# Optimization experiments

Measured on AMD Instinct MI355X. Metric: run time of the kernel, lower is better.

The kernel has to match this reference:

```python
import jax, jax.numpy as jnp
from jax import lax
import numpy as np

KSIZE = 3      # match-patch size
STRIDE = 1
RATE = 2       # down/up-sampling rate
FUSE_K = 3
SCALE = 10.0   # softmax scale
DN = ('NHWC', 'HWIO', 'NHWC')


def extract_patches(x, k, s):
    """tf.image.extract_patches(..., padding='SAME'); returns [B, L, k, k, C]."""
    B, H, W, C = x.shape
    oh, ow = -(-H // s), -(-W // s)
    ph = max((oh - 1) * s + k - H, 0)
    pw = max((ow - 1) * s + k - W, 0)
    xp = jnp.pad(x, ((0, 0), (ph // 2, ph - ph // 2), (pw // 2, pw - pw // 2), (0, 0)))
    cols = [xp[:, i:i + oh * s:s, j:j + ow * s:s, :] for i in range(k) for j in range(k)]
    p = jnp.stack(cols, axis=3)                 # [B, oh, ow, k*k, C]
    return p.reshape(B, oh * ow, k, k, C)


def setup_inputs() -> dict:
    key = jax.random.key(0)
    k1, k2, k3 = jax.random.split(key, 3)
    B, H, W, C = 4, 96, 96, 64
    f = jax.random.normal(k1, (B, H, W, C), jnp.float32)
    b = jax.random.normal(k2, (B, H, W, C), jnp.float32)
    mask = jnp.zeros((B, H, W, 1), jnp.float32)          # 0 = no hole -> all patches valid
    fuse_weight = jax.random.normal(k3, (FUSE_K, FUSE_K, 1, 1), jnp.float32) * 0.3
    return {"f": f, "b": b, "mask": mask, "fuse_weight": fuse_weight}


def reference(f, b, mask, fuse_weight):
    B, H, W, C = f.shape
    kernel = 2 * RATE
    # deconv kernels from full-res background: [B, 4, 4, C, L]
    raw_w = extract_patches(b, kernel, RATE * STRIDE).transpose(0, 2, 3, 4, 1)
    fd = f[:, 1::2, 1::2, :]
    bd = b[:, 1::2, 1::2, :]
    md = mask[:, 1::2, 1::2, :]
    h, w_ = fd.shape[1], fd.shape[2]
    L = h * w_
    # matching kernels from downscaled background: [B, 3, 3, C, L]
    wk = extract_patches(bd, KSIZE, STRIDE).transpose(0, 2, 3, 4, 1)
    # mask patches -> per-patch validity mm: [B, L]
    mp = extract_patches(md, KSIZE, STRIDE)
    mm = (jnp.mean(mp, axis=(2, 3, 4)) == 0.0).astype(f.dtype)

    def per_sample(xi, wi, rwi, mmi):
        # xi: [h, w, C]; wi: [3,3,C,L]; rwi: [4,4,C,L]; mmi: [L]
        norm = jnp.maximum(jnp.sqrt(jnp.sum(wi * wi, axis=(0, 1, 2))), 1e-4)
        yi = lax.conv_general_dilated(xi[None], wi / norm, (1, 1), 'SAME',
                                      dimension_numbers=DN)[0]        # [h, w, L]
        # fuse: 3x3 conv over flattened [HW, HW] score map, twice (transposed view)
        y = yi.reshape(1, L, L, 1)
        y = lax.conv_general_dilated(y, fuse_weight, (1, 1), 'SAME', dimension_numbers=DN)
        y = y.reshape(h, w_, h, w_).transpose(1, 0, 3, 2).reshape(1, L, L, 1)
        y = lax.conv_general_dilated(y, fuse_weight, (1, 1), 'SAME', dimension_numbers=DN)
        y = y.reshape(w_, h, w_, h).transpose(1, 0, 3, 2).reshape(h, w_, L)
        # mask-gated scaled softmax over background patches
        y = y * mmi
        y = jax.nn.softmax(y * SCALE, axis=-1) * mmi
        # deconv-style combine with raw 4x4 patches, stride=rate
        out = lax.conv_transpose(y[None], rwi, (RATE, RATE), 'SAME',
                                 dimension_numbers=DN, transpose_kernel=True)[0] / 4.0
        return out                                                    # [H, W, C]

    return jax.vmap(per_sample)(fd, wk, raw_w, mm)
```

## Files before the change

kernel.cpp:

```cpp
#include <hip/hip_runtime.h>
#include <hip/hip_bf16.h>

#define KL  2304
#define KC  64
#define KHS 48
#define KHH 96
#define OFFY (KHS*(KL + 1))

typedef __attribute__((ext_vector_type(8))) short bf16x8;
typedef __attribute__((ext_vector_type(4))) short bf16x4;
typedef __attribute__((ext_vector_type(8))) _Float16 f16x8;
typedef __attribute__((ext_vector_type(4))) _Float16 f16x4;
typedef __attribute__((ext_vector_type(4))) float f32x4;

static __device__ inline unsigned short f2bf(float x) {
    __hip_bfloat16 h = __float2bfloat16(x);
    return *reinterpret_cast<unsigned short*>(&h);
}
static __device__ inline float bf2f(unsigned short u) {
    unsigned v = ((unsigned)u) << 16;
    return __uint_as_float(v);
}
static __device__ inline unsigned short f2h(float x) {
    _Float16 h = (_Float16)x;
    return *reinterpret_cast<unsigned short*>(&h);
}
static __device__ inline float h2f(unsigned short u) {
    _Float16 h = *reinterpret_cast<_Float16*>(&u);
    return (float)h;
}

__global__ __launch_bounds__(64) void k_prep2(const float* __restrict__ f,
    const float* __restrict__ bsrc, const float* __restrict__ mask,
    float* __restrict__ nbuf, float* __restrict__ mdd,
    unsigned short* __restrict__ Ahat, unsigned short* __restrict__ Bhat)
{
    int blk = blockIdx.x;
    int p = blk % KL, bi = blk / KL;
    int y = p / KHS, x = p % KHS;
    int fy = 2*y + 1;
    int c = threadIdx.x;
    unsigned short* Ap = Ahat + ((size_t)bi*KL + p)*192;
    unsigned short* Bp = Bhat + ((size_t)bi*KL + p)*192;
    float bc = 0.f;
    #pragma unroll
    for (int dxi = 0; dxi < 3; dxi++) {
        int xx = x + dxi - 1;
        float av = 0.f, bv = 0.f;
        if ((unsigned)xx < KHS) {
            int fxx = 2*xx + 1;
            size_t src = (((size_t)bi*KHH + fy)*KHH + fxx)*KC + c;
            av = f[src]; bv = bsrc[src];
        }
        if (dxi == 1) bc = bv;
        Ap[dxi*64 + c] = f2h(av);
        Bp[dxi*64 + c] = f2h(bv);
    }
    float s = bc*bc;
    #pragma unroll
    for (int off = 32; off > 0; off >>= 1) s += __shfl_down(s, off);
    if (c == 0) {
        nbuf[bi*KL + p] = s;
        mdd[bi*KL + p]  = mask[((size_t)bi*KHH + fy)*KHH + (2*x + 1)];
    }
}

__global__ __launch_bounds__(256) void k_normmask(const float* __restrict__ nbuf,
    const float* __restrict__ mdd, float* __restrict__ rnrm, float* __restrict__ mm)
{
    int i = blockIdx.x*256 + threadIdx.x;
    int q = i % KL, bi = i / KL;
    int v = q / KHS, u = q % KHS;
    float sn = 0.f, sm = 0.f;
    for (int dy = -1; dy <= 1; dy++) {
        int vv = v + dy; if ((unsigned)vv >= KHS) continue;
        for (int dx = -1; dx <= 1; dx++) {
            int uu = u + dx; if ((unsigned)uu >= KHS) continue;
            sn += nbuf[bi*KL + vv*KHS + uu];
            sm += mdd[bi*KL + vv*KHS + uu];
        }
    }
    rnrm[i] = 1.0f / fmaxf(sqrtf(sn), 1e-4f);
    mm[i]   = (sm == 0.0f) ? 1.0f : 0.0f;
}

template<int KITERS, int OUTMODE, bool INFP16>
__global__ __launch_bounds__(256) void k_mfma_bt(const unsigned short* __restrict__ A,
    const unsigned short* __restrict__ B, void* __restrict__ Cv,
    int Ncols, size_t sA, size_t sB, size_t sC, int KDIM, int nsplit, size_t psize)
{
    int flat = blockIdx.x + gridDim.x*(blockIdx.y + gridDim.y*blockIdx.z);
    int nxy = gridDim.x*gridDim.y;
    int per = (nxy*gridDim.z) >> 3;
    int g = (flat & 7)*per + (flat >> 3);
    int z = g / nxy; int r = g - z*nxy;
    int by = r / gridDim.x; int bx = r - by*gridDim.x;

    int ks = z % nsplit, bi = z / nsplit;
    int kbase = ks * KITERS * 32;
    int n0 = bx*128, m0 = by*128;
    const unsigned short* Ab = A + (size_t)bi*sA;
    const unsigned short* Bb = B + (size_t)bi*sB;
    __shared__ unsigned short As[128*32];
    __shared__ unsigned short Bs[128*32];
    int t = threadIdx.x;
    int lane = t & 63, w = t >> 6;
    int l15 = lane & 15, quad = lane >> 4;
    int swf = (l15 >> 2) & 3;
    int wm = (w >> 1)*64, wn = (w & 1)*64;
    int srow = lane >> 2;
    int ch = lane & 3;
    f32x4 acc[4][4];
    #pragma unroll
    for (int i = 0; i < 4; i++)
        #pragma unroll
        for (int j = 0; j < 4; j++) acc[i][j] = (f32x4){0.f,0.f,0.f,0.f};

    for (int kk = 0; kk < KITERS; kk++) {
        int k0 = kbase + kk*32;
        #pragma unroll
        for (int i = 0; i < 2; i++) {
            int rbase = w*32 + i*16;
            int r2 = rbase + srow;
            int cs = (ch ^ ((r2 >> 2) & 3))*8;
            const unsigned short* ga = &Ab[(size_t)(m0 + r2)*KDIM + k0 + cs];
            __builtin_amdgcn_global_load_lds(
                (const __attribute__((address_space(1))) void*)ga,
                (__attribute__((address_space(3))) void*)&As[rbase*32], 16, 0, 0);
            const unsigned short* gb = &Bb[(size_t)(n0 + r2)*KDIM + k0 + cs];
            __builtin_amdgcn_global_load_lds(
                (const __attribute__((address_space(1))) void*)gb,
                (__attribute__((address_space(3))) void*)&Bs[rbase*32], 16, 0, 0);
        }
        __syncthreads();
        if (INFP16) {
            f16x8 af[4], bfr[4];
            #pragma unroll
            for (int mi = 0; mi < 4; mi++)
                af[mi] = *(const f16x8*)&As[(wm + mi*16 + l15)*32 + ((quad ^ swf)*8)];
            #pragma unroll
            for (int ni = 0; ni < 4; ni++)
                bfr[ni] = *(const f16x8*)&Bs[(wn + ni*16 + l15)*32 + ((quad ^ swf)*8)];
            #pragma unroll
            for (int mi = 0; mi < 4; mi++)
                #pragma unroll
                for (int ni = 0; ni < 4; ni++)
                    acc[mi][ni] = __builtin_amdgcn_mfma_f32_16x16x32_f16(
                        af[mi], bfr[ni], acc[mi][ni], 0, 0, 0);
        } else {
            bf16x8 af[4], bfr[4];
            #pragma unroll
            for (int mi = 0; mi < 4; mi++)
                af[mi] = *(const bf16x8*)&As[(wm + mi*16 + l15)*32 + ((quad ^ swf)*8)];
            #pragma unroll
            for (int ni = 0; ni < 4; ni++)
                bfr[ni] = *(const bf16x8*)&Bs[(wn + ni*16 + l15)*32 + ((quad ^ swf)*8)];
            #pragma unroll
            for (int mi = 0; mi < 4; mi++)
                #pragma unroll
                for (int ni = 0; ni < 4; ni++)
                    acc[mi][ni] = __builtin_amdgcn_mfma_f32_16x16x32_bf16(
                        af[mi], bfr[ni], acc[mi][ni], 0, 0, 0);
        }
        __syncthreads();
    }
    if (OUTMODE == 1 || OUTMODE == 2) {
        unsigned short* Cb = (unsigned short*)Cv + (size_t)ks*psize + (size_t)bi*sC;
        #pragma unroll
        for (int mi = 0; mi < 4; mi++)
            #pragma unroll
            for (int ni = 0; ni < 4; ni++) {
                int col = n0 + wn + ni*16 + l15;
                #pragma unroll
                for (int r2 = 0; r2 < 4; r2++) {
                    int row = m0 + wm + mi*16 + quad*4 + r2;
                    Cb[(size_t)row*Ncols + col] = (OUTMODE == 1)
                        ? f2bf(acc[mi][ni][r2]) : f2h(acc[mi][ni][r2]);
                }
            }
    } else {
        float* Cb = (float*)Cv + (size_t)ks*psize + (size_t)bi*sC;
        #pragma unroll
        for (int mi = 0; mi < 4; mi++)
            #pragma unroll
            for (int ni = 0; ni < 4; ni++) {
                int col = n0 + wn + ni*16 + l15;
                #pragma unroll
                for (int r2 = 0; r2 < 4; r2++) {
                    int row = m0 + wm + mi*16 + quad*4 + r2;
                    Cb[(size_t)row*Ncols + col] = acc[mi][ni][r2];
                }
            }
    }
}

#define STGA4(tt, j) do {                                                      \
    __builtin_amdgcn_global_load_lds(                                          \
        (const __attribute__((address_space(1))) void*)(gA + (size_t)(j)*128*2304 + (size_t)(tt)*32), \
        (__attribute__((address_space(3))) void*)&Atile[(tt)&3][((j)*128 + (w<<4))*32], 16, 0, 0); \
} while (0)
#define STGB4(tt, j) do {                                                      \
    __builtin_amdgcn_global_load_lds(                                          \
        (const __attribute__((address_space(1))) void*)(gB + (size_t)(j)*128*2304 + (size_t)(tt)*32), \
        (__attribute__((address_space(3))) void*)&Btile[(tt)&3][((j)*128 + (w<<4))*32], 16, 0, 0); \
} while (0)

#define MFMA_B(a, b, c) __builtin_amdgcn_mfma_f32_16x16x32_bf16(a, b, c, 0, 0, 0)

#define KT_BODY(kt, BVU, BVF) do {                                             \
    const unsigned short* At = &Atile[(kt) & 3][0];                            \
                                                          \
    __builtin_amdgcn_s_barrier();                                              \
    _Pragma("unroll")                                                          \
    for (int i = 0; i < 4; i++)                                                \
        af1[i] = *(const bf16x8*)&At[aOff + 2048 + i*512];                     \
    if ((kt) + 3 < 24) { STGA4((kt)+3, 0); STGA4((kt)+3, 1); }                 \
    __builtin_amdgcn_s_setprio(1);                                             \
    _Pragma("unroll")                                                          \
    for (int mi = 0; mi < 4; mi++)                                             \
        _Pragma("unroll")                                                      \
        for (int ni = 0; ni < 4; ni++)                                         \
            acc[mi][ni] = MFMA_B(af0[mi], BVU[ni], acc[mi][ni]);               \
    __builtin_amdgcn_s_setprio(0);                                             \
                                                          \
    __builtin_amdgcn_s_barrier();                                              \
    if ((kt) < 23) {                                                           \
        if ((kt) <= 20)      asm volatile("s_waitcnt vmcnt(6)" ::: "memory");  \
        else if ((kt) == 21) asm volatile("s_waitcnt vmcnt(4)" ::: "memory");  \
        else                 asm volatile("s_waitcnt vmcnt(0)" ::: "memory");  \
        __builtin_amdgcn_sched_barrier(0);                                     \
        const unsigned short* An = &Atile[((kt)+1) & 3][0];                    \
        const unsigned short* Bn = &Btile[((kt)+1) & 3][0];                    \
        _Pragma("unroll")                                                      \
        for (int i = 0; i < 4; i++)                                            \
            af0[i] = *(const bf16x8*)&An[aOff + i*512];                        \
        _Pragma("unroll")                                                      \
        for (int ni = 0; ni < 4; ni++)                                         \
            BVF[ni] = *(const bf16x8*)&Bn[bOff + ni*512];                      \
    }                                                                          \
    if ((kt) + 3 < 24) { STGB4((kt)+3, 0); STGB4((kt)+3, 1); }                 \
    __builtin_amdgcn_s_setprio(1);                                             \
    _Pragma("unroll")                                                          \
    for (int mi = 0; mi < 4; mi++)                                             \
        _Pragma("unroll")                                                      \
        for (int ni = 0; ni < 4; ni++)                                         \
            acc[4+mi][ni] = MFMA_B(af1[mi], BVU[ni], acc[4+mi][ni]);           \
    __builtin_amdgcn_s_setprio(0);                                             \
} while (0)

__global__ __launch_bounds__(512, 2) void k_p8(
    const unsigned short* __restrict__ A,
    const unsigned short* __restrict__ B,
    unsigned short* __restrict__ C,
    size_t psize)
{
    __shared__ unsigned short Atile[4][8192];
    __shared__ unsigned short Btile[4][8192];

    int flat = blockIdx.x + gridDim.x*(blockIdx.y + gridDim.y*blockIdx.z);
    int nwg = gridDim.x*gridDim.y*gridDim.z;
    int qq = nwg >> 3, rr8 = nwg & 7;
    int xcd = flat & 7, sub = flat >> 3;
    int g = (xcd < rr8 ? xcd*(qq+1) : rr8*(qq+1) + (xcd - rr8)*qq) + sub;
    int nxy = gridDim.x*gridDim.y;
    int z = g / nxy; int rg = g - z*nxy;
    int by = rg / gridDim.x; int bx = rg - by*gridDim.x;

    int ks = z % 3, bi = z / 3;
    int kbase = ks * 768;
    int m0 = by * 256, n0 = bx * 256;
    const unsigned short* Ab = A + (size_t)bi * (2304ull*2304);
    const unsigned short* Bb = B + (size_t)bi * (1024ull*2304);

    int t = threadIdx.x;
    int w = t >> 6, lane = t & 63;
    int wr = w >> 2, wc = w & 3;
    int l15 = lane & 15, quad = lane >> 4;

    const unsigned short* gA = Ab + (size_t)(m0 + (t >> 2))*2304 + kbase + (t & 3)*8;
    const unsigned short* gB = Bb + (size_t)(n0 + (t >> 2))*2304 + kbase + (t & 3)*8;

    int aOff = (wr*128 + l15)*32 + quad*8;
    int bOff = (wc*64  + l15)*32 + quad*8;

    f32x4 acc[8][4];
    #pragma unroll
    for (int mi = 0; mi < 8; mi++)
        #pragma unroll
        for (int ni = 0; ni < 4; ni++) acc[mi][ni] = (f32x4){0.f,0.f,0.f,0.f};

    #pragma unroll
    for (int tt = 0; tt < 3; tt++) {
        STGA4(tt, 0); STGA4(tt, 1);
        STGB4(tt, 0); STGB4(tt, 1);
    }
    asm volatile("s_waitcnt vmcnt(8)" ::: "memory");
    __builtin_amdgcn_s_barrier();

    bf16x8 af0[4], af1[4], bvA[4], bvB[4];
    #pragma unroll
    for (int i = 0; i < 4; i++)
        af0[i] = *(const bf16x8*)&Atile[0][aOff + i*512];
    #pragma unroll
    for (int ni = 0; ni < 4; ni++)
        bvA[ni] = *(const bf16x8*)&Btile[0][bOff + ni*512];

    #pragma unroll 1
    for (int ktp = 0; ktp < 12; ktp++) {
        int kt0 = ktp*2;
        KT_BODY(kt0,     bvA, bvB);
        KT_BODY(kt0 + 1, bvB, bvA);
    }

    unsigned short* Cb = C + (size_t)ks*psize + (size_t)bi*(2304ull*1024);
    #pragma unroll
    for (int mi = 0; mi < 8; mi++)
        #pragma unroll
        for (int ni = 0; ni < 4; ni++) {
            int col = n0 + wc*64 + ni*16 + l15;
            int rowb = m0 + wr*128 + mi*16 + quad*4;
            #pragma unroll
            for (int r = 0; r < 4; r++)
                Cb[(size_t)(rowb + r)*1024 + col] = f2bf(acc[mi][ni][r]);
        }
}

__global__ __launch_bounds__(256) void k_fuse_a2(const unsigned short* __restrict__ T,
    const float* __restrict__ rnrm, const float* __restrict__ fw,
    unsigned short* __restrict__ Y1)
{
    __shared__ float Sl[10][280];
    int bi = blockIdx.z;
    int qt = blockIdx.x;
    int p0 = blockIdx.y*8, q0 = qt*256;
    const unsigned short* Tb = T + (size_t)bi*KL*KL;
    const float* rn = rnrm + bi*KL;
    int t = threadIdx.x;
    bool edge = (qt == 0) | (qt == 8);
    if (!edge) {
        for (int idx = t; idx < 10*34; idx += 256) {
            int r = idx / 34, j = idx - r*34;
            int pp = p0 - 1 + r;
            int qq0 = q0 - 8 + j*8;
            float s[8];
            #pragma unroll
            for (int k = 0; k < 8; k++) s[k] = 0.f;
            if ((unsigned)pp < KL) {
                size_t base = (size_t)pp*KL + qq0;
                bool bm = (pp >= KHS), bp = (pp < KL - KHS);
                size_t offm = bm ? (size_t)OFFY : 0;
                size_t offp = bp ? (size_t)OFFY : 0;
                float fm = bm ? 1.f : 0.f, fp2 = bp ? 1.f : 0.f;
                f16x8 v0 = *(const f16x8*)&Tb[base];
                f16x8 vm = *(const f16x8*)&Tb[base - offm];
                f16x8 vp = *(const f16x8*)&Tb[base + offp];
                #pragma unroll
                for (int k = 0; k < 8; k++)
                    s[k] = ((float)v0[k] + fm*(float)vm[k] + fp2*(float)vp[k]) * rn[qq0 + k];
            }
            #pragma unroll
            for (int k = 0; k < 8; k++) Sl[r][j*8 + k] = s[k];
        }
    } else {
        for (int idx = t; idx < 10*272; idx += 256) {
            int r = idx / 272, c = idx - r*272;
            int pp = p0 - 1 + r, qq = q0 - 8 + c;
            float s = 0.f;
            if ((unsigned)pp < KL && (unsigned)qq < KL) {
                size_t base = (size_t)pp*KL + qq;
                float acc = h2f(Tb[base]);
                if (pp >= KHS && qq >= KHS)         acc += h2f(Tb[base - OFFY]);
                if (pp < KL - KHS && qq < KL - KHS) acc += h2f(Tb[base + OFFY]);
                s = acc * rn[qq];
            }
            Sl[r][c] = s;
        }
    }
    __syncthreads();
    float w[9];
    #pragma unroll
    for (int i = 0; i < 9; i++) w[i] = fw[i];
    int q = q0 + t;
    float h0[10], h1[10], h2[10];
    #pragma unroll
    for (int r = 0; r < 10; r++) {
        float s0 = Sl[r][t+7], s1 = Sl[r][t+8], s2 = Sl[r][t+9];
        h0[r] = w[0]*s0 + w[1]*s1 + w[2]*s2;
        h1[r] = w[3]*s0 + w[4]*s1 + w[5]*s2;
        h2[r] = w[6]*s0 + w[7]*s1 + w[8]*s2;
    }
    #pragma unroll
    for (int rr = 0; rr < 8; rr++) {
        Y1[((size_t)bi*KL + p0 + rr)*KL + q] = f2h(h0[rr] + h1[rr+1] + h2[rr+2]);
    }
}

__global__ __launch_bounds__(256) void k_fuse_b(const unsigned short* __restrict__ Y1,
    const float* __restrict__ fw, const float* __restrict__ mm,
    unsigned short* __restrict__ Ybf)
{
    __shared__ float rowb[4][KL];
    __shared__ float red[8];
    int blk = blockIdx.x;
    int tp0 = (blk % 1152)*2;
    int bi  = blk / 1152;
    int t = threadIdx.x;
    const unsigned short* Yb = Y1 + (size_t)bi*KL*KL;
    #pragma unroll
    for (int a = 0; a < 4; a++) {
        int t2 = tp0 - 1 + a;
        if ((unsigned)t2 < KL) {
            int pr = (t2 % KHS)*KHS + t2/KHS;
            const f16x8* src = (const f16x8*)&Yb[(size_t)pr*KL];
            for (int i = t; i < KL/8; i += 256) {
                f16x8 v = src[i];
                #pragma unroll
                for (int j = 0; j < 8; j++) rowb[a][i*8 + j] = (float)v[j];
            }
        } else {
            float4 z = {0.f,0.f,0.f,0.f};
            float4* dst = (float4*)&rowb[a][0];
            for (int i = t; i < KL/4; i += 256) dst[i] = z;
        }
    }
    float w9[9];
    #pragma unroll
    for (int i = 0; i < 9; i++) w9[i] = fw[i];
    __syncthreads();
    int w = t >> 6, lane = t & 63;
    int half = w >> 1;
    int l128 = t & 127;
    int tp = tp0 + half;
    int x = tp / KHS, y = tp - x*KHS;
    int p = y*KHS + x;
    const float* mmb = mm + bi*KL;
    float vals[18];
    float lmax = -1e30f;
    #pragma unroll
    for (int i = 0; i < 18; i++) {
        int q = l128 + i*128;
        int qm = (q >= KHS)      ? q - KHS : 2255 + q;
        int qp = (q <= KL-1-KHS) ? q + KHS : q - 2255;
        float fm = (q != 0)    ? 1.f : 0.f;
        float fp = (q != KL-1) ? 1.f : 0.f;
        float am = w9[0]*rowb[half][qm] + w9[3]*rowb[half+1][qm] + w9[6]*rowb[half+2][qm];
        float a0 = w9[1]*rowb[half][q]  + w9[4]*rowb[half+1][q]  + w9[7]*rowb[half+2][q];
        float ap = w9[2]*rowb[half][qp] + w9[5]*rowb[half+1][qp] + w9[8]*rowb[half+2][qp];
        float val = (fm*am + a0 + fp*ap) * mmb[q] * 10.0f;
        vals[i] = val;
        lmax = fmaxf(lmax, val);
    }
    #pragma unroll
    for (int off = 32; off > 0; off >>= 1) lmax = fmaxf(lmax, __shfl_down(lmax, off));
    if (lane == 0) red[w] = lmax;
    __syncthreads();
    lmax = fmaxf(red[half*2], red[half*2 + 1]);
    float lsum = 0.f;
    #pragma unroll
    for (int i = 0; i < 18; i++) {
        float e = __expf(vals[i] - lmax);
        vals[i] = e;
        lsum += e;
    }
    #pragma unroll
    for (int off = 32; off > 0; off >>= 1) lsum += __shfl_down(lsum, off);
    if (lane == 0) red[4 + w] = lsum;
    __syncthreads();
    lsum = red[4 + half*2] + red[4 + half*2 + 1];
    float inv = 1.0f / lsum;
    unsigned short* orow = Ybf + ((size_t)bi*KL + p)*KL;
    #pragma unroll
    for (int i = 0; i < 18; i++) {
        int q = l128 + i*128;
        orow[q] = f2bf(vals[i]*inv*mmb[q]);
    }
}

__global__ __launch_bounds__(256) void k_buildRt(const float* __restrict__ bsrc,
    unsigned short* __restrict__ Rt)
{
    int idx = blockIdx.x*256 + threadIdx.x;
    int k8 = idx % 288;
    int rest = idx / 288;
    int n  = rest % 1024;
    int bi = rest / 1024;
    int jj = n >> 6, c = n & 63;
    int ky = jj >> 2, kx = jj & 3;
    int k0 = k8*8;
    bf16x8 vv;
    #pragma unroll
    for (int j = 0; j < 8; j++) {
        int q = k0 + j;
        int v = q / KHS, u = q % KHS;
        int ry = 2*v + ky - 1, rx = 2*u + kx - 1;
        float val = 0.f;
        if ((unsigned)ry < KHH && (unsigned)rx < KHH)
            val = bsrc[(((size_t)bi*KHH + ry)*KHH + rx)*KC + c];
        vv[j] = (short)f2bf(val);
    }
    *(bf16x8*)&Rt[((size_t)bi*1024 + n)*KL + k0] = vv;
}

__global__ __launch_bounds__(256) void k_overlap(const unsigned short* __restrict__ P,
    float* __restrict__ out, size_t psize)
{
    size_t gid = (size_t)blockIdx.x*256 + threadIdx.x;
    int c4 = (int)(gid & 15)*4;
    size_t r = gid >> 4;
    int ix = (int)(r % KHH); r /= KHH;
    int iy = (int)(r % KHH);
    int bi = (int)(r / KHH);
    f32x4 acc = (f32x4){0.f,0.f,0.f,0.f};
    #pragma unroll
    for (int sy = 0; sy < 2; sy++) {
        int ky = (iy & 1) ? (sy*2) : (sy*2 + 1);
        int yp = (iy + 1 - ky) >> 1;
        if ((unsigned)yp >= KHS) continue;
        #pragma unroll
        for (int sx = 0; sx < 2; sx++) {
            int kx = (ix & 1) ? (sx*2) : (sx*2 + 1);
            int xp = (ix + 1 - kx) >> 1;
            if ((unsigned)xp >= KHS) continue;
            size_t idx = (((size_t)bi*KL + yp*KHS + xp)*16 + (ky*4 + kx))*64 + c4;
            #pragma unroll
            for (int s = 0; s < 3; s++) {
                bf16x4 v = *(const bf16x4*)&P[idx + s*psize];
                #pragma unroll
                for (int j = 0; j < 4; j++)
                    acc[j] += bf2f((unsigned short)v[j]);
            }
        }
    }
    f32x4 o = acc * 0.25f;
    *(f32x4*)&out[(((size_t)bi*KHH + iy)*KHH + ix)*KC + c4] = o;
}

extern "C" void kernel_launch(void* const* d_in, const int* in_sizes, int n_in,
                              void* d_out, int out_size, void* d_ws, size_t ws_size,
                              hipStream_t stream)
{
    const float* f    = (const float*)d_in[0];
    const float* b    = (const float*)d_in[1];
    const float* mask = (const float*)d_in[2];
    const float* fw   = (const float*)d_in[3];
    float* out = (float*)d_out;

    auto need = [](int nbc) -> size_t {
        return (size_t)nbc * (2ull*KL*KC + 4ull*KL + 2ull*(size_t)KL*KL) * 4ull;
    };
    int nbc = 4;
    if (need(nbc) > ws_size) nbc = 2;
    if (need(nbc) > ws_size) nbc = 1;

    for (int bi0 = 0; bi0 < 4; bi0 += nbc) {
        int nb = (4 - bi0 < nbc) ? (4 - bi0) : nbc;
        const float* fc = f    + (size_t)bi0*KHH*KHH*KC;
        const float* bc = b    + (size_t)bi0*KHH*KHH*KC;
        const float* mc = mask + (size_t)bi0*KHH*KHH;
        float* outc = out + (size_t)bi0*KHH*KHH*KC;

        float* w    = (float*)d_ws;
        float* nbuf = w;  w += (size_t)nbc*KL;
        float* mdd  = w;  w += (size_t)nbc*KL;
        float* rnrm = w;  w += (size_t)nbc*KL;
        float* mmb  = w;  w += (size_t)nbc*KL;
        float* bufA = w;  w += (size_t)nbc*KL*KL;
        float* bufB = w;
        unsigned short* Ahat = (unsigned short*)bufB;
        unsigned short* Bhat = Ahat + (size_t)nbc*KL*192;
        unsigned short* Tbuf = (unsigned short*)bufA;
        unsigned short* Y1   = (unsigned short*)bufB;
        unsigned short* Ybf = (unsigned short*)bufA;
        unsigned short* Rtb = Ybf + (size_t)nbc*KL*KL;
        unsigned short* Pbuf = (unsigned short*)bufB;
        size_t psize = (size_t)nbc*KL*1024;

        k_prep2     <<<nb*KL, 64, 0, stream>>>(fc, bc, mc, nbuf, mdd, Ahat, Bhat);
        k_normmask  <<<(nb*KL)/256, 256, 0, stream>>>(nbuf, mdd, rnrm, mmb);
        k_mfma_bt<6,2,true><<<dim3(18, 18, nb), 256, 0, stream>>>(
            Ahat, Bhat, Tbuf, KL, (size_t)KL*192, (size_t)KL*192, (size_t)KL*KL,
            192, 1, 0);
        k_fuse_a2   <<<dim3(9, 288, nb), 256, 0, stream>>>(Tbuf, rnrm, fw, Y1);
        k_fuse_b    <<<nb*1152, 256, 0, stream>>>(Y1, fw, mmb, Ybf);
        k_buildRt   <<<(nb*1024*288)/256, 256, 0, stream>>>(bc, Rtb);
        k_p8<<<dim3(4, 9, nb*3), 512, 0, stream>>>(Ybf, Rtb, Pbuf, psize);
        k_overlap   <<<nb*KL/4*16/16, 256, 0, stream>>>(Pbuf, outc, psize);
    }
}
```

Measured before the change: 284.0 us.

## Retune split-K GEMM, swizzle LDS tiles, remap blocks to XCDs, widen softmax

```diff
diff --git a/kernel.cpp b/kernel.cpp
--- a/kernel.cpp
+++ b/kernel.cpp
@@ -194,6 +194,7 @@
     }
 }
 
+#define KP_NT 18
 #define STGA4(tt, j) do {                                                      \
     __builtin_amdgcn_global_load_lds(                                          \
         (const __attribute__((address_space(1))) void*)(gA + (size_t)(j)*128*2304 + (size_t)(tt)*32), \
@@ -214,7 +215,7 @@
     _Pragma("unroll")                                                          \
     for (int i = 0; i < 4; i++)                                                \
         af1[i] = *(const bf16x8*)&At[aOff + 2048 + i*512];                     \
-    if ((kt) + 3 < 24) { STGA4((kt)+3, 0); STGA4((kt)+3, 1); }                 \
+    if ((kt) + 3 < KP_NT) { STGA4((kt)+3, 0); STGA4((kt)+3, 1); }              \
     __builtin_amdgcn_s_setprio(1);                                             \
     _Pragma("unroll")                                                          \
     for (int mi = 0; mi < 4; mi++)                                             \
@@ -224,10 +225,10 @@
     __builtin_amdgcn_s_setprio(0);                                             \
                                                           \
     __builtin_amdgcn_s_barrier();                                              \
-    if ((kt) < 23) {                                                           \
-        if ((kt) <= 20)      asm volatile("s_waitcnt vmcnt(6)" ::: "memory");  \
-        else if ((kt) == 21) asm volatile("s_waitcnt vmcnt(4)" ::: "memory");  \
-        else                 asm volatile("s_waitcnt vmcnt(0)" ::: "memory");  \
+    if ((kt) < KP_NT-1) {                                                      \
+        if ((kt) <= KP_NT-4)      asm volatile("s_waitcnt vmcnt(6)" ::: "memory"); \
+        else if ((kt) == KP_NT-3) asm volatile("s_waitcnt vmcnt(4)" ::: "memory"); \
+        else                      asm volatile("s_waitcnt vmcnt(0)" ::: "memory"); \
         __builtin_amdgcn_sched_barrier(0);                                     \
         const unsigned short* An = &Atile[((kt)+1) & 3][0];                    \
         const unsigned short* Bn = &Btile[((kt)+1) & 3][0];                    \
@@ -238,7 +239,7 @@
         for (int ni = 0; ni < 4; ni++)                                         \
             BVF[ni] = *(const bf16x8*)&Bn[bOff + ni*512];                      \
     }                                                                          \
-    if ((kt) + 3 < 24) { STGB4((kt)+3, 0); STGB4((kt)+3, 1); }                 \
+    if ((kt) + 3 < KP_NT) { STGB4((kt)+3, 0); STGB4((kt)+3, 1); }              \
     __builtin_amdgcn_s_setprio(1);                                             \
     _Pragma("unroll")                                                          \
     for (int mi = 0; mi < 4; mi++)                                             \
@@ -259,15 +260,14 @@
 
     int flat = blockIdx.x + gridDim.x*(blockIdx.y + gridDim.y*blockIdx.z);
     int nwg = gridDim.x*gridDim.y*gridDim.z;
-    int qq = nwg >> 3, rr8 = nwg & 7;
-    int xcd = flat & 7, sub = flat >> 3;
-    int g = (xcd < rr8 ? xcd*(qq+1) : rr8*(qq+1) + (xcd - rr8)*qq) + sub;
+    int cpx = nwg >> 3;
+    int g = (flat & 7)*cpx + (flat >> 3);
     int nxy = gridDim.x*gridDim.y;
     int z = g / nxy; int rg = g - z*nxy;
     int by = rg / gridDim.x; int bx = rg - by*gridDim.x;
 
-    int ks = z % 3, bi = z / 3;
-    int kbase = ks * 768;
+    int ks = z & 3, bi = z >> 2;
+    int kbase = ks * 576;
     int m0 = by * 256, n0 = bx * 256;
     const unsigned short* Ab = A + (size_t)bi * (2304ull*2304);
     const unsigned short* Bb = B + (size_t)bi * (1024ull*2304);
@@ -277,11 +277,13 @@
     int wr = w >> 2, wc = w & 3;
     int l15 = lane & 15, quad = lane >> 4;
 
-    const unsigned short* gA = Ab + (size_t)(m0 + (t >> 2))*2304 + kbase + (t & 3)*8;
-    const unsigned short* gB = Bb + (size_t)(n0 + (t >> 2))*2304 + kbase + (t & 3)*8;
-
-    int aOff = (wr*128 + l15)*32 + quad*8;
-    int bOff = (wc*64  + l15)*32 + quad*8;
+    int scol = ((t & 3) ^ ((t >> 3) & 3))*8;
+    const unsigned short* gA = Ab + (size_t)(m0 + (t >> 2))*2304 + kbase + scol;
+    const unsigned short* gB = Bb + (size_t)(n0 + (t >> 2))*2304 + kbase + scol;
+
+    int csw = (quad ^ ((l15 >> 1) & 3))*8;
+    int aOff = (wr*128 + l15)*32 + csw;
+    int bOff = (wc*64  + l15)*32 + csw;
 
     f32x4 acc[8][4];
     #pragma unroll
@@ -306,7 +308,7 @@
         bvA[ni] = *(const bf16x8*)&Btile[0][bOff + ni*512];
 
     #pragma unroll 1
-    for (int ktp = 0; ktp < 12; ktp++) {
+    for (int ktp = 0; ktp < KP_NT/2; ktp++) {
         int kt0 = ktp*2;
         KT_BODY(kt0,     bvA, bvB);
         KT_BODY(kt0 + 1, bvB, bvA);
@@ -330,9 +332,14 @@
     unsigned short* __restrict__ Y1)
 {
     __shared__ float Sl[10][280];
-    int bi = blockIdx.z;
-    int qt = blockIdx.x;
-    int p0 = blockIdx.y*8, q0 = qt*256;
+    int flat = blockIdx.x + 9*(blockIdx.y + 288*blockIdx.z);
+    int nwg = 2592*gridDim.z;
+    int cpx = nwg >> 3;
+    int g = (flat & 7)*cpx + (flat >> 3);
+    int bi = g / 2592; int rem = g - bi*2592;
+    int by = rem / 9;  int qt = rem - by*9;
+
+    int p0 = by*8, q0 = qt*256;
     const unsigned short* Tb = T + (size_t)bi*KL*KL;
     const float* rn = rnrm + bi*KL;
     int t = threadIdx.x;
@@ -399,28 +406,23 @@
     const float* __restrict__ fw, const float* __restrict__ mm,
     unsigned short* __restrict__ Ybf)
 {
-    __shared__ float rowb[4][KL];
-    __shared__ float red[8];
+    __shared__ float rowb[6][KL];
     int blk = blockIdx.x;
-    int tp0 = (blk % 1152)*2;
-    int bi  = blk / 1152;
+    int tp0 = (blk % 576)*4;
+    int bi  = blk / 576;
     int t = threadIdx.x;
     const unsigned short* Yb = Y1 + (size_t)bi*KL*KL;
-    #pragma unroll
-    for (int a = 0; a < 4; a++) {
+    for (int idx = t; idx < 6*(KL/8); idx += 256) {
+        int a = idx / (KL/8), i = idx - a*(KL/8);
         int t2 = tp0 - 1 + a;
         if ((unsigned)t2 < KL) {
             int pr = (t2 % KHS)*KHS + t2/KHS;
-            const f16x8* src = (const f16x8*)&Yb[(size_t)pr*KL];
-            for (int i = t; i < KL/8; i += 256) {
-                f16x8 v = src[i];
-                #pragma unroll
-                for (int j = 0; j < 8; j++) rowb[a][i*8 + j] = (float)v[j];
-            }
+            f16x8 v = *(const f16x8*)&Yb[(size_t)pr*KL + i*8];
+            #pragma unroll
+            for (int j = 0; j < 8; j++) rowb[a][i*8 + j] = (float)v[j];
         } else {
-            float4 z = {0.f,0.f,0.f,0.f};
-            float4* dst = (float4*)&rowb[a][0];
-            for (int i = t; i < KL/4; i += 256) dst[i] = z;
+            #pragma unroll
+            for (int j = 0; j < 8; j++) rowb[a][i*8 + j] = 0.f;
         }
     }
     float w9[9];
@@ -428,50 +430,44 @@
     for (int i = 0; i < 9; i++) w9[i] = fw[i];
     __syncthreads();
     int w = t >> 6, lane = t & 63;
-    int half = w >> 1;
-    int l128 = t & 127;
-    int tp = tp0 + half;
+    int tp = tp0 + w;
     int x = tp / KHS, y = tp - x*KHS;
     int p = y*KHS + x;
     const float* mmb = mm + bi*KL;
-    float vals[18];
+    float vals[36];
     float lmax = -1e30f;
     #pragma unroll
-    for (int i = 0; i < 18; i++) {
-        int q = l128 + i*128;
+    for (int i = 0; i < 36; i++) {
+        int q = lane + i*64;
         int qm = (q >= KHS)      ? q - KHS : 2255 + q;
         int qp = (q <= KL-1-KHS) ? q + KHS : q - 2255;
         float fm = (q != 0)    ? 1.f : 0.f;
         float fp = (q != KL-1) ? 1.f : 0.f;
-        float am = w9[0]*rowb[half][qm] + w9[3]*rowb[half+1][qm] + w9[6]*rowb[half+2][qm];
-        float a0 = w9[1]*rowb[half][q]  + w9[4]*rowb[half+1][q]  + w9[7]*rowb[half+2][q];
-        float ap = w9[2]*rowb[half][qp] + w9[5]*rowb[half+1][qp] + w9[8]*rowb[half+2][qp];
+        float am = w9[0]*rowb[w][qm] + w9[3]*rowb[w+1][qm] + w9[6]*rowb[w+2][qm];
+        float a0 = w9[1]*rowb[w][q]  + w9[4]*rowb[w+1][q]  + w9[7]*rowb[w+2][q];
+        float ap = w9[2]*rowb[w][qp] + w9[5]*rowb[w+1][qp] + w9[8]*rowb[w+2][qp];
         float val = (fm*am + a0 + fp*ap) * mmb[q] * 10.0f;
         vals[i] = val;
         lmax = fmaxf(lmax, val);
     }
     #pragma unroll
     for (int off = 32; off > 0; off >>= 1) lmax = fmaxf(lmax, __shfl_down(lmax, off));
-    if (lane == 0) red[w] = lmax;
-    __syncthreads();
-    lmax = fmaxf(red[half*2], red[half*2 + 1]);
+    lmax = __shfl(lmax, 0);
     float lsum = 0.f;
     #pragma unroll
-    for (int i = 0; i < 18; i++) {
+    for (int i = 0; i < 36; i++) {
         float e = __expf(vals[i] - lmax);
         vals[i] = e;
         lsum += e;
     }
     #pragma unroll
     for (int off = 32; off > 0; off >>= 1) lsum += __shfl_down(lsum, off);
-    if (lane == 0) red[4 + w] = lsum;
-    __syncthreads();
-    lsum = red[4 + half*2] + red[4 + half*2 + 1];
+    lsum = __shfl(lsum, 0);
     float inv = 1.0f / lsum;
     unsigned short* orow = Ybf + ((size_t)bi*KL + p)*KL;
     #pragma unroll
-    for (int i = 0; i < 18; i++) {
-        int q = l128 + i*128;
+    for (int i = 0; i < 36; i++) {
+        int q = lane + i*64;
         orow[q] = f2bf(vals[i]*inv*mmb[q]);
     }
 }
@@ -523,7 +519,7 @@
             if ((unsigned)xp >= KHS) continue;
             size_t idx = (((size_t)bi*KL + yp*KHS + xp)*16 + (ky*4 + kx))*64 + c4;
             #pragma unroll
-            for (int s = 0; s < 3; s++) {
+            for (int s = 0; s < 4; s++) {
                 bf16x4 v = *(const bf16x4*)&P[idx + s*psize];
                 #pragma unroll
                 for (int j = 0; j < 4; j++)
@@ -581,9 +577,9 @@
             Ahat, Bhat, Tbuf, KL, (size_t)KL*192, (size_t)KL*192, (size_t)KL*KL,
             192, 1, 0);
         k_fuse_a2   <<<dim3(9, 288, nb), 256, 0, stream>>>(Tbuf, rnrm, fw, Y1);
-        k_fuse_b    <<<nb*1152, 256, 0, stream>>>(Y1, fw, mmb, Ybf);
+        k_fuse_b    <<<nb*576, 256, 0, stream>>>(Y1, fw, mmb, Ybf);
         k_buildRt   <<<(nb*1024*288)/256, 256, 0, stream>>>(bc, Rtb);
-        k_p8<<<dim3(4, 9, nb*3), 512, 0, stream>>>(Ybf, Rtb, Pbuf, psize);
+        k_p8<<<dim3(4, 9, nb*4), 512, 0, stream>>>(Ybf, Rtb, Pbuf, psize);
         k_overlap   <<<nb*KL/4*16/16, 256, 0, stream>>>(Pbuf, outc, psize);
     }
 }
```

After: 281.8 us. About the same (-0.8%).
